# Kernel optimization log

Measured on AMD Instinct MI355X. Metric: run time of the kernel, lower is better.

## Reference

```python
import jax, jax.numpy as jnp
import numpy as np

B, S, D, H, DFF, NB = 32, 512, 256, 8, 1024, 2
L = NB + 2 * NB  # 2 blocks_1 + 4 blocks_2 = 6 layers, params stacked on axis 0
DK = D // H
NEG = jnp.float32(-1e32)


def _ln(x, s, b):
    mu = jnp.mean(x, -1, keepdims=True)
    var = jnp.mean((x - mu) ** 2, -1, keepdims=True)
    return (x - mu) * jax.lax.rsqrt(var + 1e-5) * s + b


def _attn(q, k, v, gamma, mask, zero_pad):
    # q,k,v: [B,H,S,DK]; mask: [1,1,S,S] bool; gamma: [H,1,1]
    scores = jnp.einsum('bhid,bhjd->bhij', q, k) / jnp.float32(np.sqrt(DK))
    # distance-decay effect (computed with no grad in the original)
    sc = jax.nn.softmax(jnp.where(mask, scores, NEG), axis=-1) * mask
    cum = jnp.cumsum(sc, axis=-1)
    tot = jnp.sum(sc, axis=-1, keepdims=True)
    idx = jnp.arange(S, dtype=jnp.float32)
    pos = jnp.abs(idx[None, :] - idx[:, None])[None, None]  # |i-j|
    dist = jax.lax.stop_gradient(jnp.sqrt(jnp.maximum((tot - cum) * pos, 0.0)))
    g = -jax.nn.softplus(gamma)[None]  # [1,H,1,1]
    eff = jnp.clip(jnp.exp(dist * g), 1e-5, 1e5)
    scores = jnp.where(mask, scores * eff, NEG)
    a = jax.nn.softmax(scores, axis=-1)
    if zero_pad:
        a = a.at[:, :, 0, :].set(0.0)
    return jnp.einsum('bhij,bhjd->bhid', a, v)


def _layer(i, mask_flag, q, k, v, apply_pos,
           Wk, bk, Wv, bv, Wo, bo, gammas, ln1_s, ln1_b, W1, b1, W2, b2, ln2_s, ln2_b):
    diag = 0 if mask_flag == 1 else -1  # mask=1: incl. diag; mask=0: strictly past
    mask = jnp.tril(jnp.ones((S, S), bool), diag)[None, None]
    to_h = lambda x, W, bb: (x @ W + bb).reshape(B, S, H, DK).transpose(0, 2, 1, 3)
    qh = to_h(q, Wk[i], bk[i])  # kq_same=True -> q uses k_linear
    kh = to_h(k, Wk[i], bk[i])
    vh = to_h(v, Wv[i], bv[i])
    o = _attn(qh, kh, vh, gammas[i], mask, zero_pad=(mask_flag == 0))
    o = o.transpose(0, 2, 1, 3).reshape(B, S, D) @ Wo[i] + bo[i]
    q = _ln(q + o, ln1_s[i], ln1_b[i])
    if apply_pos:
        f = jax.nn.relu(q @ W1[i] + b1[i]) @ W2[i] + b2[i]
        q = _ln(q + f, ln2_s[i], ln2_b[i])
    return q


def _forward(q_embed_data, qa_embed_data, *p):
    y, x = qa_embed_data, q_embed_data
    for i in range(NB):
        y = _layer(i, 1, y, y, y, True, *p)
    flag = True
    for j in range(2 * NB):
        i = NB + j
        if flag:
            x = _layer(i, 1, x, x, x, False, *p)
        else:
            x = _layer(i, 0, x, x, y, True, *p)
        flag = not flag
    return x


def setup_inputs() -> dict:
    key = jax.random.key(0)
    ks = jax.random.split(key, 9)
    sd = jnp.float32(1.0 / np.sqrt(D))
    sdf = jnp.float32(1.0 / np.sqrt(DFF))
    xb = float(np.sqrt(3.0))  # xavier bound for gammas (fan_in=fan_out=1)
    return {
        'q_embed_data': jax.random.normal(ks[0], (B, S, D), jnp.float32),
        'qa_embed_data': jax.random.normal(ks[1], (B, S, D), jnp.float32),
        'Wk': jax.random.normal(ks[2], (L, D, D), jnp.float32) * sd,
        'bk': jnp.zeros((L, D), jnp.float32),
        'Wv': jax.random.normal(ks[3], (L, D, D), jnp.float32) * sd,
        'bv': jnp.zeros((L, D), jnp.float32),
        'Wo': jax.random.normal(ks[4], (L, D, D), jnp.float32) * sd,
        'bo': jnp.zeros((L, D), jnp.float32),
        'gammas': jax.random.uniform(ks[5], (L, H, 1, 1), jnp.float32, -xb, xb),
        'ln1_s': jnp.ones((L, D), jnp.float32),
        'ln1_b': jnp.zeros((L, D), jnp.float32),
        'W1': jax.random.normal(ks[6], (L, D, DFF), jnp.float32) * sd,
        'b1': jnp.zeros((L, DFF), jnp.float32),
        'W2': jax.random.normal(ks[7], (L, DFF, D), jnp.float32) * sdf,
        'b2': jnp.zeros((L, D), jnp.float32),
        'ln2_s': jnp.ones((L, D), jnp.float32),
        'ln2_b': jnp.zeros((L, D), jnp.float32),
    }


def reference(q_embed_data, qa_embed_data, Wk, bk, Wv, bv, Wo, bo, gammas,
              ln1_s, ln1_b, W1, b1, W2, b2, ln2_s, ln2_b):
    return _forward(q_embed_data, qa_embed_data, Wk, bk, Wv, bv, Wo, bo, gammas,
                    ln1_s, ln1_b, W1, b1, W2, b2, ln2_s, ln2_b)
```

## Files before the change

kernel.cpp:

```cpp
#include <hip/hip_runtime.h>
#include <cstdint>
#include <cstddef>


#define AS1 __attribute__((address_space(1)))
#define AS3 __attribute__((address_space(3)))

typedef __bf16 bf16;
typedef __bf16 bf16x8 __attribute__((ext_vector_type(8)));
typedef __bf16 bf16x4 __attribute__((ext_vector_type(4)));
typedef __bf16 bf16x2 __attribute__((ext_vector_type(2)));
typedef float  f32x4  __attribute__((ext_vector_type(4)));
typedef float  f32x16 __attribute__((ext_vector_type(16)));
typedef unsigned int u32;

static constexpr int Mc = 32 * 512;

__global__ void cvt_copy2_kernel(const float* __restrict__ s0, float* __restrict__ da32,
                                 bf16* __restrict__ da16, const float* __restrict__ s1,
                                 float* __restrict__ db32, bf16* __restrict__ db16, int n4) {
  const float* s = blockIdx.y ? s1 : s0;
  float* d32 = blockIdx.y ? db32 : da32;
  bf16* d16 = blockIdx.y ? db16 : da16;
  int i = blockIdx.x * blockDim.x + threadIdx.x;
  if (i < n4) {
    float4 v = ((const float4*)s)[i];
    ((float4*)d32)[i] = v;
    bf16x4 hx = {(bf16)v.x, (bf16)v.y, (bf16)v.z, (bf16)v.w};
    ((bf16x4*)d16)[i] = hx;
  }
}

__global__ __launch_bounds__(256) void transpose_cvt_all(
    const float* __restrict__ Wk, const float* __restrict__ Wv, const float* __restrict__ Wo,
    const float* __restrict__ W1, const float* __restrict__ W2,
    bf16* __restrict__ Wkt, bf16* __restrict__ Wvt, bf16* __restrict__ Wot,
    bf16* __restrict__ W1t, bf16* __restrict__ W2t) {
  int z = blockIdx.z;
  int layer = z % 6, w = z / 6;
  const float* src; bf16* dst; int K, N;
  switch (w) {
    case 0: src = Wk; dst = Wkt; K = 256; N = 256; break;
    case 1: src = Wv; dst = Wvt; K = 256; N = 256; break;
    case 2: src = Wo; dst = Wot; K = 256; N = 256; break;
    case 3: src = W1; dst = W1t; K = 256; N = 1024; break;
    default: src = W2; dst = W2t; K = 1024; N = 256; break;
  }
  int k0 = blockIdx.x * 64, n0 = blockIdx.y * 64;
  if (k0 >= K || n0 >= N) return;
  src += (size_t)layer * K * N;
  dst += (size_t)layer * K * N;
  __shared__ bf16 t[64][68];
  int tid = threadIdx.x;
  int rr = tid >> 4;
  int c4 = (tid & 15) * 4;
#pragma unroll
  for (int p = 0; p < 4; ++p) {
    int k = rr + p * 16;
    float4 v = *(const float4*)(src + (size_t)(k0 + k) * N + n0 + c4);
    t[c4 + 0][k] = (bf16)v.x;
    t[c4 + 1][k] = (bf16)v.y;
    t[c4 + 2][k] = (bf16)v.z;
    t[c4 + 3][k] = (bf16)v.w;
  }
  __syncthreads();
#pragma unroll
  for (int p = 0; p < 4; ++p) {
    int nl = rr + p * 16;
    bf16x4 o4 = *(const bf16x4*)&t[nl][c4];
    *(bf16x4*)(dst + (size_t)(n0 + nl) * K + k0 + c4) = o4;
  }
}

template <int RELU, typename OUT_T>
__device__ __forceinline__ void gemm_body(
    const bf16* __restrict__ A, const bf16* __restrict__ Bt,
    const float* __restrict__ bias, OUT_T* __restrict__ C,
    int K, int N, int m0, int n0, bf16* As, bf16* Bs) {
  const int tid = threadIdx.x;
  const int lane = tid & 63;
  const int wid = tid >> 6;
  const int wm = (wid >> 1) * 64;
  const int wn = (wid & 1) * 64;
  f32x4 acc[4][4] = {};

  const int o1 = wid * 1024 + lane * 16;
  const int o2 = o1 + 4096;
  const int r1 = o1 >> 6, c1 = o1 & 63;
  const int r2 = o2 >> 6, c2 = o2 & 63;
  const char* Ab = (const char*)A;
  const char* Bb = (const char*)Bt;
  const size_t stride = (size_t)K * 2;

  for (int k0 = 0; k0 < K; k0 += 32) {
    const char* a1 = Ab + (size_t)(m0 + r1) * stride + (size_t)k0 * 2 + c1;
    const char* a2 = Ab + (size_t)(m0 + r2) * stride + (size_t)k0 * 2 + c2;
    const char* b1 = Bb + (size_t)(n0 + r1) * stride + (size_t)k0 * 2 + c1;
    const char* b2 = Bb + (size_t)(n0 + r2) * stride + (size_t)k0 * 2 + c2;
    __builtin_amdgcn_global_load_lds((const AS1 u32*)a1, (AS3 u32*)((char*)As + wid * 1024), 16, 0, 0);
    __builtin_amdgcn_global_load_lds((const AS1 u32*)a2, (AS3 u32*)((char*)As + wid * 1024 + 4096), 16, 0, 0);
    __builtin_amdgcn_global_load_lds((const AS1 u32*)b1, (AS3 u32*)((char*)Bs + wid * 1024), 16, 0, 0);
    __builtin_amdgcn_global_load_lds((const AS1 u32*)b2, (AS3 u32*)((char*)Bs + wid * 1024 + 4096), 16, 0, 0);
    asm volatile("s_waitcnt vmcnt(0)" ::: "memory");
    __syncthreads();

    const int rr = lane & 15;
    const int g8 = (lane >> 4) * 8;
    bf16x8 af[4], bfr[4];
#pragma unroll
    for (int i = 0; i < 4; ++i) {
      af[i]  = *(const bf16x8*)&As[(wm + i * 16 + rr) * 32 + g8];
      bfr[i] = *(const bf16x8*)&Bs[(wn + i * 16 + rr) * 32 + g8];
    }
#pragma unroll
    for (int mi = 0; mi < 4; ++mi)
#pragma unroll
      for (int ni = 0; ni < 4; ++ni)
        acc[mi][ni] = __builtin_amdgcn_mfma_f32_16x16x32_bf16(af[mi], bfr[ni], acc[mi][ni], 0, 0, 0);
    __syncthreads();
  }

  const int rr = lane & 15;
  const int g4 = (lane >> 4) * 4;
  float bv[4];
#pragma unroll
  for (int ni = 0; ni < 4; ++ni) bv[ni] = bias[n0 + wn + ni * 16 + rr];
#pragma unroll
  for (int mi = 0; mi < 4; ++mi)
#pragma unroll
    for (int ni = 0; ni < 4; ++ni)
#pragma unroll
      for (int r = 0; r < 4; ++r) {
        float v = acc[mi][ni][r] + bv[ni];
        if (RELU) v = fmaxf(v, 0.f);
        int row = m0 + wm + mi * 16 + g4 + r;
        int col = n0 + wn + ni * 16 + rr;
        C[(size_t)row * N + col] = (OUT_T)v;
      }
}

template <int RELU, typename OUT_T>
__global__ __launch_bounds__(256) void gemm_bias_kernel(
    const bf16* __restrict__ A, const bf16* __restrict__ Bt,
    const float* __restrict__ bias, OUT_T* __restrict__ C, int K, int N) {
  __shared__ bf16 As[128 * 32];
  __shared__ bf16 Bs[128 * 32];
  gemm_body<RELU, OUT_T>(A, Bt, bias, C, K, N, blockIdx.x * 128, blockIdx.y * 128, As, Bs);
}

__global__ __launch_bounds__(256) void gemm_kv_kernel(
    const bf16* __restrict__ A0, const bf16* __restrict__ Bt0,
    const float* __restrict__ b0, bf16* __restrict__ C0,
    const bf16* __restrict__ A1, const bf16* __restrict__ Bt1,
    const float* __restrict__ b1, bf16* __restrict__ C1, int K, int N) {
  __shared__ bf16 As[128 * 32];
  __shared__ bf16 Bs[128 * 32];
  int sel = blockIdx.y >> 1;
  gemm_body<0, bf16>(sel ? A1 : A0, sel ? Bt1 : Bt0, sel ? b1 : b0, sel ? C1 : C0,
                     K, N, blockIdx.x * 128, (blockIdx.y & 1) * 128, As, Bs);
}

template <int KSZ>
__global__ __launch_bounds__(512, 4) void gemm_ln_kernel(
    const bf16* __restrict__ A, const bf16* __restrict__ Bt,
    const float* __restrict__ bias, const float* __restrict__ resid,
    const float* __restrict__ lns, const float* __restrict__ lnb,
    float* __restrict__ out32, bf16* __restrict__ out16) {
  __shared__ bf16 As[32 * 32];
  __shared__ bf16 Bs[256 * 32];
  __shared__ float wsum[8][16][2];
  __shared__ float stats[32][2];
  const int tid = threadIdx.x, lane = tid & 63, wid = tid >> 6;
  const int m0 = blockIdx.x * 32;
  const int wr = wid >> 2, wc = wid & 3;
  f32x4 acc[4] = {};
  const char* Ab = (const char*)A;
  const char* Bb = (const char*)Bt;
  const size_t stride = (size_t)KSZ * 2;

  for (int k0 = 0; k0 < KSZ; k0 += 32) {
    if (wid < 2) {
      int off = wid * 1024 + lane * 16;
      const char* a1 = Ab + (size_t)(m0 + (off >> 6)) * stride + (size_t)k0 * 2 + (off & 63);
      __builtin_amdgcn_global_load_lds((const AS1 u32*)a1, (AS3 u32*)((char*)As + wid * 1024), 16, 0, 0);
    }
    {
      int off1 = wid * 2048 + lane * 16;
      int off2 = off1 + 1024;
      const char* b1 = Bb + (size_t)(off1 >> 6) * stride + (size_t)k0 * 2 + (off1 & 63);
      const char* b2 = Bb + (size_t)(off2 >> 6) * stride + (size_t)k0 * 2 + (off2 & 63);
      __builtin_amdgcn_global_load_lds((const AS1 u32*)b1, (AS3 u32*)((char*)Bs + wid * 2048), 16, 0, 0);
      __builtin_amdgcn_global_load_lds((const AS1 u32*)b2, (AS3 u32*)((char*)Bs + wid * 2048 + 1024), 16, 0, 0);
    }
    asm volatile("s_waitcnt vmcnt(0)" ::: "memory");
    __syncthreads();
    const int rr = lane & 15, g8 = (lane >> 4) * 8;
    bf16x8 af = *(const bf16x8*)&As[(wr * 16 + rr) * 32 + g8];
    bf16x8 bfr[4];
#pragma unroll
    for (int ni = 0; ni < 4; ++ni)
      bfr[ni] = *(const bf16x8*)&Bs[(wc * 64 + ni * 16 + rr) * 32 + g8];
#pragma unroll
    for (int ni = 0; ni < 4; ++ni)
      acc[ni] = __builtin_amdgcn_mfma_f32_16x16x32_bf16(af, bfr[ni], acc[ni], 0, 0, 0);
    __syncthreads();
  }

  const int rr = lane & 15, g4 = (lane >> 4) * 4;
  float bv[4], scv[4], biv[4];
  int col[4];
#pragma unroll
  for (int ni = 0; ni < 4; ++ni) {
    col[ni] = wc * 64 + ni * 16 + rr;
    bv[ni] = bias[col[ni]];
    scv[ni] = lns[col[ni]];
    biv[ni] = lnb[col[ni]];
  }
  float v[4][4];
#pragma unroll
  for (int r = 0; r < 4; ++r) {
    int grow = m0 + wr * 16 + g4 + r;
#pragma unroll
    for (int ni = 0; ni < 4; ++ni)
      v[ni][r] = acc[ni][r] + bv[ni] + resid[(size_t)grow * 256 + col[ni]];
  }
#pragma unroll
  for (int r = 0; r < 4; ++r) {
    float s1 = (v[0][r] + v[1][r]) + (v[2][r] + v[3][r]);
    float s2 = (v[0][r] * v[0][r] + v[1][r] * v[1][r]) + (v[2][r] * v[2][r] + v[3][r] * v[3][r]);
#pragma unroll
    for (int off = 8; off; off >>= 1) {
      s1 += __shfl_xor(s1, off);
      s2 += __shfl_xor(s2, off);
    }
    if (rr == 0) {
      int lrow = wr * 16 + g4 + r;
      wsum[wid][lrow & 15][0] = s1;
      wsum[wid][lrow & 15][1] = s2;
    }
  }
  __syncthreads();
  if (tid < 32) {
    int row = tid;
    int band = row >> 4;
    float s1 = 0.f, s2 = 0.f;
#pragma unroll
    for (int k = 0; k < 4; ++k) {
      s1 += wsum[band * 4 + k][row & 15][0];
      s2 += wsum[band * 4 + k][row & 15][1];
    }
    float mu = s1 * (1.f / 256.f);
    float var = s2 * (1.f / 256.f) - mu * mu;
    stats[row][0] = mu;
    stats[row][1] = rsqrtf(var + 1e-5f);
  }
  __syncthreads();
#pragma unroll
  for (int r = 0; r < 4; ++r) {
    int lrow = wr * 16 + g4 + r;
    int grow = m0 + lrow;
    float mu = stats[lrow][0], rs = stats[lrow][1];
#pragma unroll
    for (int ni = 0; ni < 4; ++ni) {
      float y = (v[ni][r] - mu) * rs * scv[ni] + biv[ni];
      out32[(size_t)grow * 256 + col[ni]] = y;
      out16[(size_t)grow * 256 + col[ni]] = (bf16)y;
    }
  }
}

static constexpr int LDK = 34;
static constexpr int LDV = 534;
static constexpr float LOG2E = 1.4426950408889634f;
static constexpr float KSC = 0.17677669529663687f * LOG2E;

__device__ __forceinline__ int jloc(int r, int hi) { return (r & 3) + 8 * (r >> 2) + 4 * hi; }

__device__ __forceinline__ u32 pkbf(float x, float y) {
  bf16x2 t = {(bf16)x, (bf16)y};
  return __builtin_bit_cast(u32, t);
}

__device__ __forceinline__ void plswap(u32& a, u32& b) {
  asm volatile("v_permlane32_swap_b32 %0, %1" : "+v"(a), "+v"(b));
}

__device__ __forceinline__ f32x16 qk_tile(const bf16* Klds, int jbase, int lq,
                                          const bf16x8& qf0, const bf16x8& qf1, int hi) {
  const bf16x8 ka0 = *(const bf16x8*)&Klds[(jbase + lq) * LDK + hi * 8];
  const bf16x8 ka1 = *(const bf16x8*)&Klds[(jbase + lq) * LDK + 16 + hi * 8];
  f32x16 c = {};
  c = __builtin_amdgcn_mfma_f32_32x32x16_bf16(ka0, qf0, c, 0, 0, 0);
  c = __builtin_amdgcn_mfma_f32_32x32x16_bf16(ka1, qf1, c, 0, 0, 0);
  return c;
}

template <bool MASKED>
__device__ __forceinline__ void tileA(const f32x16& c, int jbase, int hi, int qlim, float& tot) {
  float t[4] = {0.f, 0.f, 0.f, 0.f};
#pragma unroll
  for (int q2 = 0; q2 < 4; ++q2)
#pragma unroll
    for (int p = 0; p < 4; ++p) {
      const int r = q2 * 4 + p;
      float e = __builtin_amdgcn_exp2f(c[r] * KSC);
      if (MASKED) {
        int j = jbase + 8 * q2 + 4 * hi + p;
        if (j > qlim) e = 0.f;
      }
      t[q2] += e;
    }
  tot += (t[0] + t[1]) + (t[2] + t[3]);
}

template <bool MASKED>
__device__ __forceinline__ void tileB(const f32x16& c, int jbase, int lq, int hi,
                                      int qlim, float itot, float gneg2, float posf,
                                      const bf16* Vt, float& run, float& sum2, f32x16& pvacc) {
  float su2[16], lcs[16], G[4];
#pragma unroll
  for (int q2 = 0; q2 < 4; ++q2) {
    float a = 0.f;
#pragma unroll
    for (int p = 0; p < 4; ++p) {
      const int r = q2 * 4 + p;
      su2[r] = c[r] * KSC;
      float e = __builtin_amdgcn_exp2f(su2[r]);
      if (MASKED) {
        int j = jbase + 8 * q2 + 4 * hi + p;
        if (j > qlim) e = 0.f;
      }
      a += e;
      lcs[r] = a;
    }
    G[q2] = a;
  }
  float Po[4];
#pragma unroll
  for (int q2 = 0; q2 < 4; ++q2) Po[q2] = __shfl_xor(G[q2], 32);
  float base[4];
  {
    float pre = run;
#pragma unroll
    for (int q2 = 0; q2 < 4; ++q2) {
      base[q2] = pre + (hi ? Po[q2] : 0.f);
      pre += G[q2] + Po[q2];
    }
    run = pre;
  }
#pragma unroll
  for (int cc = 0; cc < 2; ++cc) {
    float pv[8];
#pragma unroll
    for (int q2s = 0; q2s < 2; ++q2s) {
      const int q2 = cc * 2 + q2s;
#pragma unroll
      for (int p = 0; p < 4; ++p) {
        const int r = q2 * 4 + p;
        float cum = base[q2] + lcs[r];
        float pos = posf - (float)(8 * q2 + p);
        float d2 = fmaxf(__builtin_fmaf(-cum, itot, 1.f) * pos, 0.f);
        float dist = __builtin_amdgcn_sqrtf(d2);
        float eff = fmaxf(__builtin_amdgcn_exp2f(dist * gneg2), 1e-5f);
        float t = __builtin_amdgcn_exp2f(su2[r] * eff);
        if (MASKED) {
          int j = jbase + 8 * q2 + 4 * hi + p;
          if (j > qlim) t = 0.f;
        }
        pv[q2s * 4 + p] = t;
      }
    }
    sum2 += ((pv[0] + pv[1]) + (pv[2] + pv[3])) + ((pv[4] + pv[5]) + (pv[6] + pv[7]));
    u32 a0 = pkbf(pv[0], pv[1]);
    u32 a1 = pkbf(pv[2], pv[3]);
    u32 b0 = pkbf(pv[4], pv[5]);
    u32 b1 = pkbf(pv[6], pv[7]);
    plswap(a0, b0);
    plswap(a1, b1);
    uint4 fq; fq.x = a0; fq.y = a1; fq.z = b0; fq.w = b1;
    bf16x8 pa = __builtin_bit_cast(bf16x8, fq);
    bf16x8 vb = *(const bf16x8*)&Vt[(size_t)lq * LDV + jbase + cc * 16 + hi * 8];
    pvacc = __builtin_amdgcn_mfma_f32_32x32x16_bf16(pa, vb, pvacc, 0, 0, 0);
  }
}

__global__ __launch_bounds__(1024, 4) void attn_kernel(
    const bf16* __restrict__ kh, const bf16* __restrict__ vh,
    const float* __restrict__ gam, bf16* __restrict__ o, int incl_diag) {
  __shared__ bf16 Klds[512 * LDK];
  __shared__ bf16 Vt[32 * LDV];

  const int tid = threadIdx.x;
  const int lane = tid & 63;
  const int wid = tid >> 6;
  const int bh = blockIdx.x;
  const int b = bh >> 3, h = bh & 7;
  const bf16* kbase = kh + ((size_t)b * 4096 + h) * 32;
  const bf16* vbase = vh + ((size_t)b * 4096 + h) * 32;
  bf16* obase = o + ((size_t)b * 4096 + h) * 32;

#pragma unroll
  for (int it = 0; it < 2; ++it) {
    int t = it * 1024 + tid;
    int j = t >> 2, cc = t & 3;
    bf16x8 kv8 = *(const bf16x8*)(kbase + (size_t)j * 256 + cc * 8);
    *(bf16x8*)&Klds[j * LDK + cc * 8] = kv8;
  }
  {
    int u = tid & 255;
    int cg = tid >> 8;
    const bf16* vb = vbase + (size_t)(2 * u) * 256 + cg * 8;
    bf16x8 r0 = *(const bf16x8*)(vb);
    bf16x8 r1 = *(const bf16x8*)(vb + 256);
#pragma unroll
    for (int e = 0; e < 8; ++e) {
      bf16x2 w2 = {r0[e], r1[e]};
      *(bf16x2*)&Vt[(size_t)(cg * 8 + e) * LDV + 2 * u] = w2;
    }
  }
  __syncthreads();

  float gm = gam[h];
  float gneg = -(fmaxf(gm, 0.f) + log1pf(__expf(-fabsf(gm))));
  const float gneg2 = gneg * LOG2E;
  const int lq = lane & 31;
  const int hi = lane >> 5;

  const int k = wid & 3, gsel = wid >> 2;
  int qb;
  switch (gsel) {
    case 0: qb = k; break;
    case 1: qb = 7 - k; break;
    case 2: qb = 8 + k; break;
    default: qb = 15 - k; break;
  }
  const int q0 = qb * 32;
  const int qr = q0 + lq;
  const int qlim = incl_diag ? qr : qr - 1;

  const bf16x8 qf0 = *(const bf16x8*)&Klds[(q0 + lq) * LDK + hi * 8];
  const bf16x8 qf1 = *(const bf16x8*)&Klds[(q0 + lq) * LDK + 16 + hi * 8];

  float tot = 0.f;
  for (int jt = 0; jt < qb; ++jt) {
    f32x16 c = qk_tile(Klds, jt * 32, lq, qf0, qf1, hi);
    tileA<false>(c, jt * 32, hi, qlim, tot);
  }
  {
    f32x16 c = qk_tile(Klds, q0, lq, qf0, qf1, hi);
    tileA<true>(c, q0, hi, qlim, tot);
  }
  tot += __shfl_xor(tot, 32);
  const float itot = tot > 0.f ? 1.f / tot : 0.f;

  float run = 0.f, sum2 = 0.f;
  f32x16 pvacc = {};
  float posf = (float)(qr - 4 * hi);
  for (int jt = 0; jt < qb; ++jt) {
    f32x16 c = qk_tile(Klds, jt * 32, lq, qf0, qf1, hi);
    tileB<false>(c, jt * 32, lq, hi, qlim, itot, gneg2, posf, Vt, run, sum2, pvacc);
    posf -= 32.f;
  }
  {
    f32x16 c = qk_tile(Klds, q0, lq, qf0, qf1, hi);
    tileB<true>(c, q0, lq, hi, qlim, itot, gneg2, posf, Vt, run, sum2, pvacc);
  }
  sum2 += __shfl_xor(sum2, 32);
  const float inv2 = sum2 > 0.f ? 1.f / sum2 : 0.f;

#pragma unroll
  for (int r = 0; r < 16; ++r) {
    int qv = jloc(r, hi);
    float iv = __shfl(inv2, qv);
    obase[(size_t)(q0 + qv) * 256 + lq] = (bf16)(pvacc[r] * iv);
  }
}

extern "C" void kernel_launch(void* const* d_in, const int* in_sizes, int n_in,
                              void* d_out, int out_size, void* d_ws, size_t ws_size,
                              hipStream_t stream) {
  const float* q_embed  = (const float*)d_in[0];
  const float* qa_embed = (const float*)d_in[1];
  const float* Wk = (const float*)d_in[2];
  const float* bk = (const float*)d_in[3];
  const float* Wv = (const float*)d_in[4];
  const float* bv = (const float*)d_in[5];
  const float* Wo = (const float*)d_in[6];
  const float* bo = (const float*)d_in[7];
  const float* gammas = (const float*)d_in[8];
  const float* ln1_s = (const float*)d_in[9];
  const float* ln1_b = (const float*)d_in[10];
  const float* W1 = (const float*)d_in[11];
  const float* b1 = (const float*)d_in[12];
  const float* W2 = (const float*)d_in[13];
  const float* b2 = (const float*)d_in[14];
  const float* ln2_s = (const float*)d_in[15];
  const float* ln2_b = (const float*)d_in[16];
  float* out = (float*)d_out;

  char* ws = (char*)d_ws;
  float* y32 = (float*)(ws);
  float* x32 = (float*)(ws + ((size_t)16 << 20));
  bf16* y16  = (bf16*)(ws + ((size_t)32 << 20));
  bf16* x16  = (bf16*)(ws + ((size_t)40 << 20));
  bf16* khb  = (bf16*)(ws + ((size_t)48 << 20));
  bf16* vhb  = (bf16*)(ws + ((size_t)56 << 20));
  bf16* o16  = (bf16*)(ws + ((size_t)64 << 20));
  bf16* h116 = (bf16*)(ws + ((size_t)88 << 20));
  bf16* Wkt  = (bf16*)(ws + ((size_t)122 << 20));
  bf16* Wvt  = Wkt + 6 * 65536;
  bf16* Wot  = Wvt + 6 * 65536;
  bf16* W1t  = Wot + 6 * 65536;
  bf16* W2t  = W1t + 6 * 262144;

  transpose_cvt_all<<<dim3(16, 16, 30), 256, 0, stream>>>(Wk, Wv, Wo, W1, W2,
                                                          Wkt, Wvt, Wot, W1t, W2t);
  cvt_copy2_kernel<<<dim3(4096, 2), 256, 0, stream>>>(q_embed, x32, x16,
                                                      qa_embed, y32, y16, Mc * 256 / 4);

  for (int i = 0; i < 6; ++i) {
    const bool first = (i < 2);
    const bool strict = (i == 3 || i == 5);
    const bool pos = first || strict;
    bf16* in16 = first ? y16 : x16;
    bf16* v16  = (first || strict) ? y16 : x16;
    float* res32 = first ? y32 : x32;

    gemm_kv_kernel<<<dim3(128, 4), 256, 0, stream>>>(
        in16, Wkt + (size_t)i * 65536, bk + i * 256, khb,
        v16, Wvt + (size_t)i * 65536, bv + i * 256, vhb, 256, 256);
    attn_kernel<<<256, 1024, 0, stream>>>(khb, vhb, gammas + i * 8, o16, strict ? 0 : 1);
    gemm_ln_kernel<256><<<512, 512, 0, stream>>>(
        o16, Wot + (size_t)i * 65536, bo + i * 256, res32,
        ln1_s + i * 256, ln1_b + i * 256, res32, in16);
    if (pos) {
      gemm_bias_kernel<1, bf16><<<dim3(128, 8), 256, 0, stream>>>(
          in16, W1t + (size_t)i * 262144, b1 + i * 1024, h116, 256, 1024);
      float* fin = (i == 5) ? out : res32;
      gemm_ln_kernel<1024><<<512, 512, 0, stream>>>(
          h116, W2t + (size_t)i * 262144, b2 + i * 256, res32,
          ln2_s + i * 256, ln2_b + i * 256, fin, in16);
    }
  }
}
```

Before: 608.5 us.

## Double-buffer GEMM LDS tiles and software-pipeline QK tiles in attention

The GEMM and GEMM+LayerNorm kernels now use two LDS buffers, so the async global-to-LDS load of the next K-slice is issued before the MFMAs on the current slice run. This hides global load latency behind compute and drops one barrier per iteration. The attention kernel computes the next QK score tile before processing the current one, so MFMA latency overlaps the softmax and decay arithmetic. The cost is doubled LDS use, which may lower occupancy, most notably for gemm_ln at launch bounds of 4 blocks, plus higher register pressure in attention.

```diff
diff --git a/kernel.cpp b/kernel.cpp
--- a/kernel.cpp
+++ b/kernel.cpp
@@ -92,32 +92,43 @@
   const char* Bb = (const char*)Bt;
   const size_t stride = (size_t)K * 2;
 
+  auto stage = [&](int buf, int kk) {
+    const char* a1 = Ab + (size_t)(m0 + r1) * stride + (size_t)kk * 2 + c1;
+    const char* a2 = Ab + (size_t)(m0 + r2) * stride + (size_t)kk * 2 + c2;
+    const char* b1 = Bb + (size_t)(n0 + r1) * stride + (size_t)kk * 2 + c1;
+    const char* b2 = Bb + (size_t)(n0 + r2) * stride + (size_t)kk * 2 + c2;
+    char* ad = (char*)As + buf * 8192 + wid * 1024;
+    char* bd = (char*)Bs + buf * 8192 + wid * 1024;
+    __builtin_amdgcn_global_load_lds((const AS1 u32*)a1, (AS3 u32*)ad, 16, 0, 0);
+    __builtin_amdgcn_global_load_lds((const AS1 u32*)a2, (AS3 u32*)(ad + 4096), 16, 0, 0);
+    __builtin_amdgcn_global_load_lds((const AS1 u32*)b1, (AS3 u32*)bd, 16, 0, 0);
+    __builtin_amdgcn_global_load_lds((const AS1 u32*)b2, (AS3 u32*)(bd + 4096), 16, 0, 0);
+  };
+
+  stage(0, 0);
+  asm volatile("s_waitcnt vmcnt(0)" ::: "memory");
+  __syncthreads();
+
+  int cur = 0;
   for (int k0 = 0; k0 < K; k0 += 32) {
-    const char* a1 = Ab + (size_t)(m0 + r1) * stride + (size_t)k0 * 2 + c1;
-    const char* a2 = Ab + (size_t)(m0 + r2) * stride + (size_t)k0 * 2 + c2;
-    const char* b1 = Bb + (size_t)(n0 + r1) * stride + (size_t)k0 * 2 + c1;
-    const char* b2 = Bb + (size_t)(n0 + r2) * stride + (size_t)k0 * 2 + c2;
-    __builtin_amdgcn_global_load_lds((const AS1 u32*)a1, (AS3 u32*)((char*)As + wid * 1024), 16, 0, 0);
-    __builtin_amdgcn_global_load_lds((const AS1 u32*)a2, (AS3 u32*)((char*)As + wid * 1024 + 4096), 16, 0, 0);
-    __builtin_amdgcn_global_load_lds((const AS1 u32*)b1, (AS3 u32*)((char*)Bs + wid * 1024), 16, 0, 0);
-    __builtin_amdgcn_global_load_lds((const AS1 u32*)b2, (AS3 u32*)((char*)Bs + wid * 1024 + 4096), 16, 0, 0);
+    if (k0 + 32 < K) stage(cur ^ 1, k0 + 32);
+    const int rr = lane & 15;
+    const int g8 = (lane >> 4) * 8;
+    const int base = cur * 4096;
+    bf16x8 af[4], bfr[4];
+#pragma unroll
+    for (int i = 0; i < 4; ++i) {
+      af[i]  = *(const bf16x8*)&As[base + (wm + i * 16 + rr) * 32 + g8];
+      bfr[i] = *(const bf16x8*)&Bs[base + (wn + i * 16 + rr) * 32 + g8];
+    }
+#pragma unroll
+    for (int mi = 0; mi < 4; ++mi)
+#pragma unroll
+      for (int ni = 0; ni < 4; ++ni)
+        acc[mi][ni] = __builtin_amdgcn_mfma_f32_16x16x32_bf16(af[mi], bfr[ni], acc[mi][ni], 0, 0, 0);
     asm volatile("s_waitcnt vmcnt(0)" ::: "memory");
     __syncthreads();
-
-    const int rr = lane & 15;
-    const int g8 = (lane >> 4) * 8;
-    bf16x8 af[4], bfr[4];
-#pragma unroll
-    for (int i = 0; i < 4; ++i) {
-      af[i]  = *(const bf16x8*)&As[(wm + i * 16 + rr) * 32 + g8];
-      bfr[i] = *(const bf16x8*)&Bs[(wn + i * 16 + rr) * 32 + g8];
-    }
-#pragma unroll
-    for (int mi = 0; mi < 4; ++mi)
-#pragma unroll
-      for (int ni = 0; ni < 4; ++ni)
-        acc[mi][ni] = __builtin_amdgcn_mfma_f32_16x16x32_bf16(af[mi], bfr[ni], acc[mi][ni], 0, 0, 0);
-    __syncthreads();
+    cur ^= 1;
   }
 
   const int rr = lane & 15;
@@ -143,8 +154,8 @@
 __global__ __launch_bounds__(256) void gemm_bias_kernel(
     const bf16* __restrict__ A, const bf16* __restrict__ Bt,
     const float* __restrict__ bias, OUT_T* __restrict__ C, int K, int N) {
-  __shared__ bf16 As[128 * 32];
-  __shared__ bf16 Bs[128 * 32];
+  __shared__ bf16 As[2 * 128 * 32];
+  __shared__ bf16 Bs[2 * 128 * 32];
   gemm_body<RELU, OUT_T>(A, Bt, bias, C, K, N, blockIdx.x * 128, blockIdx.y * 128, As, Bs);
 }
 
@@ -153,8 +164,8 @@
     const float* __restrict__ b0, bf16* __restrict__ C0,
     const bf16* __restrict__ A1, const bf16* __restrict__ Bt1,
     const float* __restrict__ b1, bf16* __restrict__ C1, int K, int N) {
-  __shared__ bf16 As[128 * 32];
-  __shared__ bf16 Bs[128 * 32];
+  __shared__ bf16 As[2 * 128 * 32];
+  __shared__ bf16 Bs[2 * 128 * 32];
   int sel = blockIdx.y >> 1;
   gemm_body<0, bf16>(sel ? A1 : A0, sel ? Bt1 : Bt0, sel ? b1 : b0, sel ? C1 : C0,
                      K, N, blockIdx.x * 128, (blockIdx.y & 1) * 128, As, Bs);
@@ -166,8 +177,8 @@
     const float* __restrict__ bias, const float* __restrict__ resid,
     const float* __restrict__ lns, const float* __restrict__ lnb,
     float* __restrict__ out32, bf16* __restrict__ out16) {
-  __shared__ bf16 As[32 * 32];
-  __shared__ bf16 Bs[256 * 32];
+  __shared__ bf16 As[2 * 32 * 32];
+  __shared__ bf16 Bs[2 * 256 * 32];
   __shared__ float wsum[8][16][2];
   __shared__ float stats[32][2];
   const int tid = threadIdx.x, lane = tid & 63, wid = tid >> 6;
@@ -178,32 +189,41 @@
   const char* Bb = (const char*)Bt;
   const size_t stride = (size_t)KSZ * 2;
 
-  for (int k0 = 0; k0 < KSZ; k0 += 32) {
+  auto stage = [&](int buf, int kk) {
     if (wid < 2) {
       int off = wid * 1024 + lane * 16;
-      const char* a1 = Ab + (size_t)(m0 + (off >> 6)) * stride + (size_t)k0 * 2 + (off & 63);
-      __builtin_amdgcn_global_load_lds((const AS1 u32*)a1, (AS3 u32*)((char*)As + wid * 1024), 16, 0, 0);
-    }
-    {
-      int off1 = wid * 2048 + lane * 16;
-      int off2 = off1 + 1024;
-      const char* b1 = Bb + (size_t)(off1 >> 6) * stride + (size_t)k0 * 2 + (off1 & 63);
-      const char* b2 = Bb + (size_t)(off2 >> 6) * stride + (size_t)k0 * 2 + (off2 & 63);
-      __builtin_amdgcn_global_load_lds((const AS1 u32*)b1, (AS3 u32*)((char*)Bs + wid * 2048), 16, 0, 0);
-      __builtin_amdgcn_global_load_lds((const AS1 u32*)b2, (AS3 u32*)((char*)Bs + wid * 2048 + 1024), 16, 0, 0);
-    }
+      const char* a1 = Ab + (size_t)(m0 + (off >> 6)) * stride + (size_t)kk * 2 + (off & 63);
+      __builtin_amdgcn_global_load_lds((const AS1 u32*)a1,
+                                       (AS3 u32*)((char*)As + buf * 2048 + wid * 1024), 16, 0, 0);
+    }
+    int off1 = wid * 2048 + lane * 16;
+    int off2 = off1 + 1024;
+    const char* b1 = Bb + (size_t)(off1 >> 6) * stride + (size_t)kk * 2 + (off1 & 63);
+    const char* b2 = Bb + (size_t)(off2 >> 6) * stride + (size_t)kk * 2 + (off2 & 63);
+    char* bd = (char*)Bs + buf * 16384 + wid * 2048;
+    __builtin_amdgcn_global_load_lds((const AS1 u32*)b1, (AS3 u32*)bd, 16, 0, 0);
+    __builtin_amdgcn_global_load_lds((const AS1 u32*)b2, (AS3 u32*)(bd + 1024), 16, 0, 0);
+  };
+
+  stage(0, 0);
+  asm volatile("s_waitcnt vmcnt(0)" ::: "memory");
+  __syncthreads();
+
+  int cur = 0;
+  for (int k0 = 0; k0 < KSZ; k0 += 32) {
+    if (k0 + 32 < KSZ) stage(cur ^ 1, k0 + 32);
+    const int rr = lane & 15, g8 = (lane >> 4) * 8;
+    bf16x8 af = *(const bf16x8*)&As[cur * 1024 + (wr * 16 + rr) * 32 + g8];
+    bf16x8 bfr[4];
+#pragma unroll
+    for (int ni = 0; ni < 4; ++ni)
+      bfr[ni] = *(const bf16x8*)&Bs[cur * 8192 + (wc * 64 + ni * 16 + rr) * 32 + g8];
+#pragma unroll
+    for (int ni = 0; ni < 4; ++ni)
+      acc[ni] = __builtin_amdgcn_mfma_f32_16x16x32_bf16(af, bfr[ni], acc[ni], 0, 0, 0);
     asm volatile("s_waitcnt vmcnt(0)" ::: "memory");
     __syncthreads();
-    const int rr = lane & 15, g8 = (lane >> 4) * 8;
-    bf16x8 af = *(const bf16x8*)&As[(wr * 16 + rr) * 32 + g8];
-    bf16x8 bfr[4];
-#pragma unroll
-    for (int ni = 0; ni < 4; ++ni)
-      bfr[ni] = *(const bf16x8*)&Bs[(wc * 64 + ni * 16 + rr) * 32 + g8];
-#pragma unroll
-    for (int ni = 0; ni < 4; ++ni)
-      acc[ni] = __builtin_amdgcn_mfma_f32_16x16x32_bf16(af, bfr[ni], acc[ni], 0, 0, 0);
-    __syncthreads();
+    cur ^= 1;
   }
 
   const int rr = lane & 15, g4 = (lane >> 4) * 4;
@@ -442,12 +462,13 @@
   const bf16x8 qf1 = *(const bf16x8*)&Klds[(q0 + lq) * LDK + 16 + hi * 8];
 
   float tot = 0.f;
-  for (int jt = 0; jt < qb; ++jt) {
-    f32x16 c = qk_tile(Klds, jt * 32, lq, qf0, qf1, hi);
-    tileA<false>(c, jt * 32, hi, qlim, tot);
-  }
   {
-    f32x16 c = qk_tile(Klds, q0, lq, qf0, qf1, hi);
+    f32x16 c = qk_tile(Klds, 0, lq, qf0, qf1, hi);
+    for (int jt = 0; jt < qb; ++jt) {
+      f32x16 cn = qk_tile(Klds, (jt + 1) * 32, lq, qf0, qf1, hi);
+      tileA<false>(c, jt * 32, hi, qlim, tot);
+      c = cn;
+    }
     tileA<true>(c, q0, hi, qlim, tot);
   }
   tot += __shfl_xor(tot, 32);
@@ -456,13 +477,14 @@
   float run = 0.f, sum2 = 0.f;
   f32x16 pvacc = {};
   float posf = (float)(qr - 4 * hi);
-  for (int jt = 0; jt < qb; ++jt) {
-    f32x16 c = qk_tile(Klds, jt * 32, lq, qf0, qf1, hi);
-    tileB<false>(c, jt * 32, lq, hi, qlim, itot, gneg2, posf, Vt, run, sum2, pvacc);
-    posf -= 32.f;
-  }
   {
-    f32x16 c = qk_tile(Klds, q0, lq, qf0, qf1, hi);
+    f32x16 c = qk_tile(Klds, 0, lq, qf0, qf1, hi);
+    for (int jt = 0; jt < qb; ++jt) {
+      f32x16 cn = qk_tile(Klds, (jt + 1) * 32, lq, qf0, qf1, hi);
+      tileB<false>(c, jt * 32, lq, hi, qlim, itot, gneg2, posf, Vt, run, sum2, pvacc);
+      posf -= 32.f;
+      c = cn;
+    }
     tileB<true>(c, q0, lq, hi, qlim, itot, gneg2, posf, Vt, run, sum2, pvacc);
   }
   sum2 += __shfl_xor(sum2, 32);
```

New measurement: 614.7 us. Within noise of the previous version (+1.0%).
